# Optimization experiments

Hardware: AMD Instinct MI355X
Metric: run time of the kernel (lower is better)

## Reference

```python
import jax, jax.numpy as jnp
import numpy as np

L, C, B = 256, 20, 1024


def _pos_mask(L):
    # pairwise mask: l2 - l1 >= 1, shape (L, L); broadcast over channels
    ls = jnp.arange(L)
    return (ls[None, :] - ls[:, None]) >= 1


def setup_inputs() -> dict:
    key = jax.random.key(0)
    k0, k1, k2 = jax.random.split(key, 3)
    x_lc = jax.random.uniform(k0, (B, L, C), dtype=jnp.float32)
    theta_0 = jnp.zeros((1,), dtype=jnp.float32)
    theta_lc = jax.random.normal(k1, (1, L, C), dtype=jnp.float32) / np.sqrt(L)
    pm = _pos_mask(L)
    theta_lclc = (jax.random.normal(k2, (1, L, C, L, C), dtype=jnp.float32)
                  / np.sqrt(L * L)) * pm[None, :, None, :, None]
    mask = pm
    return {"x_lc": x_lc, "theta_0": theta_0, "theta_lc": theta_lc,
            "theta_lclc": theta_lclc, "mask": mask}


def reference(x_lc, theta_0, theta_lc, theta_lclc, mask):
    Bn = x_lc.shape[0]
    # additive term: sum_{l,c} theta_lc * x
    phi = theta_0 + jnp.einsum('blc,zlc->b', x_lc, theta_lc)[:, None]
    # pairwise term as a masked bilinear form: x^T (mask * theta) x
    # (avoids materializing the (B,L,C,L,C) broadcast of the original)
    theta_m = theta_lclc[0] * mask[:, None, :, None].astype(theta_lclc.dtype)
    LC = L * C
    xf = x_lc.reshape(Bn, LC)                      # (B, LC)
    tf_ = theta_m.reshape(LC, LC)                  # (LC, LC)
    pair = jnp.einsum('bi,ij,bj->b', xf, tf_, xf)  # two GEMMs under the hood
    phi = phi + pair[:, None]
    return phi
```

## Files before the change

kernel.cpp:

```cpp
#include <hip/hip_runtime.h>
#include <stdint.h>

#define LDIM 256
#define CDIM 20
#define LC   5120
#define NB   1024
#define BM   128
#define BN   256
#define ITOT64 1640

typedef __attribute__((ext_vector_type(8))) short short8;
typedef __attribute__((ext_vector_type(4))) float float4v;
typedef __attribute__((ext_vector_type(4))) unsigned int uint4v;
typedef unsigned short ushort_t;

#define TB_BYTES (52428800ull)
#define XB_BYTES (10485760ull)
#define WS_NEED  (TB_BYTES + XB_BYTES)

__device__ inline uint32_t pack_bf16x2(float a, float b) {
    uint32_t ua = __float_as_uint(a);
    uint32_t ub = __float_as_uint(b);
    ua += 0x7fffu + ((ua >> 16) & 1u);
    ub += 0x7fffu + ((ub >> 16) & 1u);
    return (ua >> 16) | (ub & 0xffff0000u);
}

__device__ inline float bf16_to_f32(ushort_t u) {
    return __uint_as_float(((uint32_t)u) << 16);
}

__device__ inline void load_lds16(const void* g, void* l) {
    __builtin_amdgcn_global_load_lds(
        (const __attribute__((address_space(1))) uint32_t*)g,
        (__attribute__((address_space(3))) uint32_t*)l, 16, 0, 0);
}

__global__ __launch_bounds__(256) void conv_kernel(
    const float* __restrict__ T, const float* __restrict__ X,
    const float* __restrict__ th0, const float* __restrict__ thlc,
    ushort_t* __restrict__ Tb, ushort_t* __restrict__ Xb,
    float* __restrict__ out)
{
    const int bid = blockIdx.x;
    const int t   = threadIdx.x;
    __shared__ float red[4];

    if (bid < LC) {
        const int r  = bid;
        const int tk = (r >> 7) << 7;
        const float*  src = T  + (size_t)r * LC;
        ushort_t*     dst = Tb + (size_t)r * LC;
        for (int c = tk + t * 4; c < LC; c += 1024) {
            float4 f = *(const float4*)(src + c);
            uint2 u;
            u.x = pack_bf16x2(f.x, f.y);
            u.y = pack_bf16x2(f.z, f.w);
            *(uint2*)(dst + c) = u;
        }
    } else {
        const int b = bid - LC;
        const float*  src = X  + (size_t)b * LC;
        ushort_t*     dst = Xb + (size_t)b * LC;
        float s = 0.f;
        for (int c = t * 4; c < LC; c += 1024) {
            float4 f = *(const float4*)(src + c);
            float4 w = *(const float4*)(thlc + c);
            s += f.x * w.x + f.y * w.y + f.z * w.z + f.w * w.w;
            uint2 u;
            u.x = pack_bf16x2(f.x, f.y);
            u.y = pack_bf16x2(f.z, f.w);
            *(uint2*)(dst + c) = u;
        }
        s += __shfl_xor(s, 1);  s += __shfl_xor(s, 2);  s += __shfl_xor(s, 4);
        s += __shfl_xor(s, 8);  s += __shfl_xor(s, 16); s += __shfl_xor(s, 32);
        if ((t & 63) == 0) red[t >> 6] = s;
        __syncthreads();
        if (t == 0) out[b] = th0[0] + red[0] + red[1] + red[2] + red[3];
    }
}

__global__ __launch_bounds__(256, 2) void pair_bf(
    const ushort_t* __restrict__ Tb, const ushort_t* __restrict__ Xb,
    float* __restrict__ out)
{
    const int n    = blockIdx.x;
    const int kblk = (n & 7) | (((n >> 5) & 15) << 3);
    const int bn0  = ((n >> 3) & 3) * BN;

    const int gbeg = (ITOT64 * kblk) >> 7;
    const int gend = (ITOT64 * (kblk + 1)) >> 7;

    int it = 0, pre = 0;
    while (pre + (80 - 2 * it) <= gbeg) { pre += 80 - 2 * it; ++it; }
    int li = gbeg - pre;

    __shared__ __align__(16) ushort_t A_s[1024 * 8];
    __shared__ __align__(16) ushort_t B_s[2048 * 8];

    const int t    = threadIdx.x;
    const int lane = t & 63;
    const int wid  = t >> 6;
    const int wm   = (wid >> 1) * 64;
    const int wn   = (wid & 1) * 128;
    const int l16  = lane & 15;
    const int qk   = lane >> 4;

    uint32_t offA[4];
    #pragma unroll
    for (int j = 0; j < 4; ++j) {
        const int c = (wid << 8) + (j << 6) + lane;
        const int row = c >> 3;
        const int g = (c & 7) ^ (row & 7);
        offA[j] = (uint32_t)row * LC + (g << 3);
    }
    uint32_t offB[8];
    #pragma unroll
    for (int j = 0; j < 8; ++j) {
        const int c = (wid << 9) + (j << 6) + lane;
        const int row = c >> 3;
        const int g = (c & 7) ^ (row & 7);
        offB[j] = (uint32_t)(bn0 + row) * LC + (g << 3);
    }

    int adrA[2][4], adrB[2][8];
    #pragma unroll
    for (int step = 0; step < 2; ++step) {
        const int kf = step * 4 + qk;
        #pragma unroll
        for (int mt = 0; mt < 4; ++mt) {
            const int r = wm + mt * 16 + l16;
            adrA[step][mt] = ((r << 3) + (kf ^ (r & 7))) << 4;
        }
        #pragma unroll
        for (int nt = 0; nt < 8; ++nt) {
            const int r = wn + nt * 16 + l16;
            adrB[step][nt] = ((r << 3) + (kf ^ (r & 7))) << 4;
        }
    }

    int   i0    = it << 7;
    int   k0    = i0 + (li << 6);
    size_t baseA = (size_t)i0 * LC + k0;

    float4v acc[4][8];
    #pragma unroll
    for (int mt = 0; mt < 4; ++mt)
        #pragma unroll
        for (int nt = 0; nt < 8; ++nt)
            #pragma unroll
            for (int r = 0; r < 4; ++r) acc[mt][nt][r] = 0.f;

    for (int g = gbeg; g < gend; ++g) {
        __syncthreads();
        #pragma unroll
        for (int j = 0; j < 4; ++j)
            load_lds16(Tb + baseA + offA[j], A_s + (((wid << 8) + (j << 6)) << 3));
        #pragma unroll
        for (int j = 0; j < 8; ++j)
            load_lds16(Xb + k0 + offB[j],   B_s + (((wid << 9) + (j << 6)) << 3));
        __syncthreads();

        #pragma unroll
        for (int step = 0; step < 2; ++step) {
            short8 af[4], bfr[8];
            #pragma unroll
            for (int mt = 0; mt < 4; ++mt)
                af[mt] = *(const short8*)((const char*)A_s + adrA[step][mt]);
            #pragma unroll
            for (int nt = 0; nt < 8; ++nt)
                bfr[nt] = *(const short8*)((const char*)B_s + adrB[step][nt]);
            #pragma unroll
            for (int mt = 0; mt < 4; ++mt)
                #pragma unroll
                for (int nt = 0; nt < 8; ++nt)
                    acc[mt][nt] = __builtin_amdgcn_mfma_f32_16x16x32_bf16(
                        af[mt], bfr[nt], acc[mt][nt], 0, 0, 0);
        }

        ++li;
        const bool segEnd = (li == 80 - 2 * it);
        if (segEnd || g + 1 == gend) {
            #pragma unroll
            for (int nt = 0; nt < 8; ++nt) {
                const int b = bn0 + wn + nt * 16 + l16;
                const ushort_t* xb = Xb + (size_t)b * LC + i0 + wm + qk * 4;
                float s = 0.f;
                #pragma unroll
                for (int mt = 0; mt < 4; ++mt) {
                    ushort4 xv = *(const ushort4*)(xb + mt * 16);
                    s += acc[mt][nt][0] * bf16_to_f32(xv.x)
                       + acc[mt][nt][1] * bf16_to_f32(xv.y)
                       + acc[mt][nt][2] * bf16_to_f32(xv.z)
                       + acc[mt][nt][3] * bf16_to_f32(xv.w);
                }
                s += __shfl_xor(s, 16);
                s += __shfl_xor(s, 32);
                if (qk == 0) atomicAdd(&out[b], s);
            }
            #pragma unroll
            for (int mt = 0; mt < 4; ++mt)
                #pragma unroll
                for (int nt = 0; nt < 8; ++nt)
                    #pragma unroll
                    for (int r = 0; r < 4; ++r) acc[mt][nt][r] = 0.f;
        }
        if (segEnd) {
            ++it; li = 0;
            if (it < 40) {
                i0 = it << 7;
                k0 = i0;
                baseA = (size_t)i0 * LC + k0;
            }
        } else {
            k0 += 64;
            baseA += 64;
        }
    }
}

__global__ __launch_bounds__(256) void init_kernel(
    const float* __restrict__ x, const float* __restrict__ th0,
    const float* __restrict__ thlc, float* __restrict__ out)
{
    const int b = blockIdx.x;
    const float4* xb = (const float4*)(x + (size_t)b * LC);
    const float4* tv = (const float4*)thlc;
    float s = 0.f;
    for (int i = threadIdx.x; i < LC / 4; i += 256) {
        float4 a = xb[i], t = tv[i];
        s += a.x * t.x + a.y * t.y + a.z * t.z + a.w * t.w;
    }
    s += __shfl_xor(s, 1);  s += __shfl_xor(s, 2);  s += __shfl_xor(s, 4);
    s += __shfl_xor(s, 8);  s += __shfl_xor(s, 16); s += __shfl_xor(s, 32);
    __shared__ float red[4];
    if ((threadIdx.x & 63) == 0) red[threadIdx.x >> 6] = s;
    __syncthreads();
    if (threadIdx.x == 0) out[b] = th0[0] + red[0] + red[1] + red[2] + red[3];
}

__global__ __launch_bounds__(256) void pair_kernel(
    const float* __restrict__ T, const float* __restrict__ X,
    float* __restrict__ out)
{
    const int n  = blockIdx.x;
    const int r  = n & 7;
    const int g  = n >> 3;
    const int i0  = (g >> 3) * BM;
    const int bn0 = (g & 7) * 128;
    const int kstart = i0;
    const int nIter  = (LC - kstart) >> 6;
    const int ipc    = (nIter + 7) >> 3;
    const int itBeg  = r * ipc;
    const int itEnd  = (itBeg + ipc < nIter) ? (itBeg + ipc) : nIter;
    if (itBeg >= itEnd) return;
    const int kbeg   = kstart + (itBeg << 6);

    __shared__ __align__(16) short A_s[8 * BM * 8];
    __shared__ __align__(16) short B_s[8 * BM * 8];

    const int t    = threadIdx.x;
    const int lane = t & 63;
    const int wid  = t >> 6;
    const int wm   = (wid >> 1) * 64;
    const int wn   = (wid & 1) * 64;
    const int l16  = lane & 15;
    const int qk   = lane >> 4;

    const float* pA[4]; const float* pB[4]; int sIdx[4];
    #pragma unroll
    for (int u = 0; u < 4; ++u) {
        const int id  = t + u * 256;
        const int row = id >> 3;
        const int kq  = id & 7;
        pA[u] = T + (size_t)(i0 + row) * LC + kbeg + kq * 8;
        pB[u] = X + (size_t)(bn0 + row) * LC + kbeg + kq * 8;
        sIdx[u] = (kq * BM + (row ^ kq)) * 8;
    }

    float4v acc[4][4] = {};
    for (int itr = itBeg; itr < itEnd; ++itr) {
        __syncthreads();
        #pragma unroll
        for (int u = 0; u < 4; ++u) {
            float4 a0 = ((const float4*)pA[u])[0];
            float4 a1 = ((const float4*)pA[u])[1];
            float4 b0 = ((const float4*)pB[u])[0];
            float4 b1 = ((const float4*)pB[u])[1];
            pA[u] += 64; pB[u] += 64;
            uint4v va, vb;
            va[0] = pack_bf16x2(a0.x, a0.y); va[1] = pack_bf16x2(a0.z, a0.w);
            va[2] = pack_bf16x2(a1.x, a1.y); va[3] = pack_bf16x2(a1.z, a1.w);
            vb[0] = pack_bf16x2(b0.x, b0.y); vb[1] = pack_bf16x2(b0.z, b0.w);
            vb[2] = pack_bf16x2(b1.x, b1.y); vb[3] = pack_bf16x2(b1.z, b1.w);
            *(uint4v*)(A_s + sIdx[u]) = va;
            *(uint4v*)(B_s + sIdx[u]) = vb;
        }
        __syncthreads();
        #pragma unroll
        for (int step = 0; step < 2; ++step) {
            const int kf = step * 4 + qk;
            short8 af[4], bfr[4];
            #pragma unroll
            for (int mt = 0; mt < 4; ++mt)
                af[mt] = *(const short8*)(A_s + (kf * BM + ((wm + mt * 16 + l16) ^ kf)) * 8);
            #pragma unroll
            for (int nt = 0; nt < 4; ++nt)
                bfr[nt] = *(const short8*)(B_s + (kf * BM + ((wn + nt * 16 + l16) ^ kf)) * 8);
            #pragma unroll
            for (int mt = 0; mt < 4; ++mt)
                #pragma unroll
                for (int nt = 0; nt < 4; ++nt)
                    acc[mt][nt] = __builtin_amdgcn_mfma_f32_16x16x32_bf16(
                        af[mt], bfr[nt], acc[mt][nt], 0, 0, 0);
        }
    }
    #pragma unroll
    for (int nt = 0; nt < 4; ++nt) {
        const int b = bn0 + wn + nt * 16 + l16;
        const float* xb = X + (size_t)b * LC + i0 + wm + qk * 4;
        float s = 0.f;
        #pragma unroll
        for (int mt = 0; mt < 4; ++mt) {
            float4 xv = *(const float4*)(xb + mt * 16);
            s += acc[mt][nt][0] * xv.x + acc[mt][nt][1] * xv.y +
                 acc[mt][nt][2] * xv.z + acc[mt][nt][3] * xv.w;
        }
        s += __shfl_xor(s, 16);
        s += __shfl_xor(s, 32);
        if (qk == 0) atomicAdd(&out[b], s);
    }
}

extern "C" void kernel_launch(void* const* d_in, const int* in_sizes, int n_in,
                              void* d_out, int out_size, void* d_ws, size_t ws_size,
                              hipStream_t stream) {
    const float* x    = (const float*)d_in[0];
    const float* th0  = (const float*)d_in[1];
    const float* thlc = (const float*)d_in[2];
    const float* T    = (const float*)d_in[3];
    float* out = (float*)d_out;

    if (ws_size >= WS_NEED) {
        ushort_t* Tb = (ushort_t*)d_ws;
        ushort_t* Xb = (ushort_t*)((char*)d_ws + TB_BYTES);
        conv_kernel<<<LC + NB, 256, 0, stream>>>(T, x, th0, thlc, Tb, Xb, out);
        pair_bf<<<512, 256, 0, stream>>>(Tb, Xb, out);
    } else {
        init_kernel<<<NB, 256, 0, stream>>>(x, th0, thlc, out);
        pair_kernel<<<(LC / BM) * (NB / 128) * 8, 256, 0, stream>>>(T, x, out);
    }
}
```

Measured before the change: 215.5 us.

## Fuse fp32-to-bf16 conversion of theta into the pairwise GEMM tile loads

Drops the separate pass that converted the theta matrix to a bf16 workspace copy. The GEMM kernel now loads fp32 theta tiles into registers, packs them to bf16 and stores them swizzled into LDS. This removes a large write and reread of the bf16 copy and shrinks the workspace. In exchange, each column block rereads fp32 data at twice the byte width, and the asynchronous direct-to-LDS loads for A are replaced by synchronous register staging.

```diff
diff --git a/kernel.cpp b/kernel.cpp
--- a/kernel.cpp
+++ b/kernel.cpp
@@ -14,9 +14,8 @@
 typedef __attribute__((ext_vector_type(4))) unsigned int uint4v;
 typedef unsigned short ushort_t;
 
-#define TB_BYTES (52428800ull)
 #define XB_BYTES (10485760ull)
-#define WS_NEED  (TB_BYTES + XB_BYTES)
+#define WS_NEED  (XB_BYTES)
 
 __device__ inline uint32_t pack_bf16x2(float a, float b) {
     uint32_t ua = __float_as_uint(a);
@@ -36,52 +35,36 @@
         (__attribute__((address_space(3))) uint32_t*)l, 16, 0, 0);
 }
 
-__global__ __launch_bounds__(256) void conv_kernel(
-    const float* __restrict__ T, const float* __restrict__ X,
-    const float* __restrict__ th0, const float* __restrict__ thlc,
-    ushort_t* __restrict__ Tb, ushort_t* __restrict__ Xb,
+__global__ __launch_bounds__(256) void xconv_kernel(
+    const float* __restrict__ X, const float* __restrict__ th0,
+    const float* __restrict__ thlc, ushort_t* __restrict__ Xb,
     float* __restrict__ out)
 {
-    const int bid = blockIdx.x;
-    const int t   = threadIdx.x;
+    const int b = blockIdx.x;
+    const int t = threadIdx.x;
     __shared__ float red[4];
 
-    if (bid < LC) {
-        const int r  = bid;
-        const int tk = (r >> 7) << 7;
-        const float*  src = T  + (size_t)r * LC;
-        ushort_t*     dst = Tb + (size_t)r * LC;
-        for (int c = tk + t * 4; c < LC; c += 1024) {
-            float4 f = *(const float4*)(src + c);
-            uint2 u;
-            u.x = pack_bf16x2(f.x, f.y);
-            u.y = pack_bf16x2(f.z, f.w);
-            *(uint2*)(dst + c) = u;
-        }
-    } else {
-        const int b = bid - LC;
-        const float*  src = X  + (size_t)b * LC;
-        ushort_t*     dst = Xb + (size_t)b * LC;
-        float s = 0.f;
-        for (int c = t * 4; c < LC; c += 1024) {
-            float4 f = *(const float4*)(src + c);
-            float4 w = *(const float4*)(thlc + c);
-            s += f.x * w.x + f.y * w.y + f.z * w.z + f.w * w.w;
-            uint2 u;
-            u.x = pack_bf16x2(f.x, f.y);
-            u.y = pack_bf16x2(f.z, f.w);
-            *(uint2*)(dst + c) = u;
-        }
-        s += __shfl_xor(s, 1);  s += __shfl_xor(s, 2);  s += __shfl_xor(s, 4);
-        s += __shfl_xor(s, 8);  s += __shfl_xor(s, 16); s += __shfl_xor(s, 32);
-        if ((t & 63) == 0) red[t >> 6] = s;
-        __syncthreads();
-        if (t == 0) out[b] = th0[0] + red[0] + red[1] + red[2] + red[3];
-    }
-}
-
-__global__ __launch_bounds__(256, 2) void pair_bf(
-    const ushort_t* __restrict__ Tb, const ushort_t* __restrict__ Xb,
+    const float*  src = X  + (size_t)b * LC;
+    ushort_t*     dst = Xb + (size_t)b * LC;
+    float s = 0.f;
+    for (int c = t * 4; c < LC; c += 1024) {
+        float4 f = *(const float4*)(src + c);
+        float4 w = *(const float4*)(thlc + c);
+        s += f.x * w.x + f.y * w.y + f.z * w.z + f.w * w.w;
+        uint2 u;
+        u.x = pack_bf16x2(f.x, f.y);
+        u.y = pack_bf16x2(f.z, f.w);
+        *(uint2*)(dst + c) = u;
+    }
+    s += __shfl_xor(s, 1);  s += __shfl_xor(s, 2);  s += __shfl_xor(s, 4);
+    s += __shfl_xor(s, 8);  s += __shfl_xor(s, 16); s += __shfl_xor(s, 32);
+    if ((t & 63) == 0) red[t >> 6] = s;
+    __syncthreads();
+    if (t == 0) out[b] = th0[0] + red[0] + red[1] + red[2] + red[3];
+}
+
+__global__ __launch_bounds__(256, 2) void pair_fused(
+    const float* __restrict__ T, const ushort_t* __restrict__ Xb,
     float* __restrict__ out)
 {
     const int n    = blockIdx.x;
@@ -106,14 +89,17 @@
     const int l16  = lane & 15;
     const int qk   = lane >> 4;
 
-    uint32_t offA[4];
+    const int r32 = t >> 3;
+    const int ga  = t & 7;
+    uint32_t offTa[4];
+    int      wAdr[4];
     #pragma unroll
     for (int j = 0; j < 4; ++j) {
-        const int c = (wid << 8) + (j << 6) + lane;
-        const int row = c >> 3;
-        const int g = (c & 7) ^ (row & 7);
-        offA[j] = (uint32_t)row * LC + (g << 3);
-    }
+        const int row = r32 + j * 32;
+        offTa[j] = (uint32_t)row * LC + (ga << 3);
+        wAdr[j]  = ((row << 3) + (ga ^ (row & 7))) << 4;
+    }
+
     uint32_t offB[8];
     #pragma unroll
     for (int j = 0; j < 8; ++j) {
@@ -139,9 +125,8 @@
         }
     }
 
-    int   i0    = it << 7;
-    int   k0    = i0 + (li << 6);
-    size_t baseA = (size_t)i0 * LC + k0;
+    int i0 = it << 7;
+    int k0 = i0 + (li << 6);
 
     float4v acc[4][8];
     #pragma unroll
@@ -153,12 +138,26 @@
 
     for (int g = gbeg; g < gend; ++g) {
         __syncthreads();
-        #pragma unroll
-        for (int j = 0; j < 4; ++j)
-            load_lds16(Tb + baseA + offA[j], A_s + (((wid << 8) + (j << 6)) << 3));
+
+        const float* Tbase = T + (size_t)i0 * LC + k0;
+        float4 a0[4], a1[4];
+        #pragma unroll
+        for (int j = 0; j < 4; ++j) {
+            a0[j] = *(const float4*)(Tbase + offTa[j]);
+            a1[j] = *(const float4*)(Tbase + offTa[j] + 4);
+        }
         #pragma unroll
         for (int j = 0; j < 8; ++j)
-            load_lds16(Xb + k0 + offB[j],   B_s + (((wid << 9) + (j << 6)) << 3));
+            load_lds16(Xb + k0 + offB[j], B_s + (((wid << 9) + (j << 6)) << 3));
+        #pragma unroll
+        for (int j = 0; j < 4; ++j) {
+            uint4v v;
+            v[0] = pack_bf16x2(a0[j].x, a0[j].y);
+            v[1] = pack_bf16x2(a0[j].z, a0[j].w);
+            v[2] = pack_bf16x2(a1[j].x, a1[j].y);
+            v[3] = pack_bf16x2(a1[j].z, a1[j].w);
+            *(uint4v*)((char*)A_s + wAdr[j]) = v;
+        }
         __syncthreads();
 
         #pragma unroll
@@ -210,11 +209,9 @@
             if (it < 40) {
                 i0 = it << 7;
                 k0 = i0;
-                baseA = (size_t)i0 * LC + k0;
             }
         } else {
             k0 += 64;
-            baseA += 64;
         }
     }
 }
@@ -342,10 +339,9 @@
     float* out = (float*)d_out;
 
     if (ws_size >= WS_NEED) {
-        ushort_t* Tb = (ushort_t*)d_ws;
-        ushort_t* Xb = (ushort_t*)((char*)d_ws + TB_BYTES);
-        conv_kernel<<<LC + NB, 256, 0, stream>>>(T, x, th0, thlc, Tb, Xb, out);
-        pair_bf<<<512, 256, 0, stream>>>(Tb, Xb, out);
+        ushort_t* Xb = (ushort_t*)d_ws;
+        xconv_kernel<<<NB, 256, 0, stream>>>(x, th0, thlc, Xb, out);
+        pair_fused<<<512, 256, 0, stream>>>(T, Xb, out);
     } else {
         init_kernel<<<NB, 256, 0, stream>>>(x, th0, thlc, out);
         pair_kernel<<<(LC / BM) * (NB / 128) * 8, 256, 0, stream>>>(T, x, out);
```

Result: faster. 205.0 us (-4.9%).

## Replace LDS-staged bf16 GEMM with direct-to-register per-wave MFMA tiles

Applied to the files above, without the earlier changes.

The bf16 pair kernel no longer stages A/B tiles through LDS with block-wide barriers. Each wave now loads MFMA fragments straight from global memory into registers and works on a 64x64 tile with its own slice of the triangular K range. The triangle granularity drops from 128 to 64 rows, so the conversion kernel skips more of the masked lower triangle. Occupancy is raised to three blocks per CU. This removes barrier and LDS overhead, but in exchange there is no data reuse across waves, more redundant global/L2 traffic, and uncoalesced 16-byte row loads.

```diff
diff --git a/kernel.cpp b/kernel.cpp
--- a/kernel.cpp
+++ b/kernel.cpp
@@ -5,13 +5,10 @@
 #define CDIM 20
 #define LC   5120
 #define NB   1024
-#define BM   128
-#define BN   256
-#define ITOT64 1640
+#define ITOT 3240
 
 typedef __attribute__((ext_vector_type(8))) short short8;
 typedef __attribute__((ext_vector_type(4))) float float4v;
-typedef __attribute__((ext_vector_type(4))) unsigned int uint4v;
 typedef unsigned short ushort_t;
 
 #define TB_BYTES (52428800ull)
@@ -28,12 +25,6 @@
 
 __device__ inline float bf16_to_f32(ushort_t u) {
     return __uint_as_float(((uint32_t)u) << 16);
-}
-
-__device__ inline void load_lds16(const void* g, void* l) {
-    __builtin_amdgcn_global_load_lds(
-        (const __attribute__((address_space(1))) uint32_t*)g,
-        (__attribute__((address_space(3))) uint32_t*)l, 16, 0, 0);
 }
 
 __global__ __launch_bounds__(256) void conv_kernel(
@@ -48,7 +39,7 @@
 
     if (bid < LC) {
         const int r  = bid;
-        const int tk = (r >> 7) << 7;
+        const int tk = (r >> 6) << 6;
         const float*  src = T  + (size_t)r * LC;
         ushort_t*     dst = Tb + (size_t)r * LC;
         for (int c = tk + t * 4; c < LC; c += 1024) {
@@ -80,111 +71,76 @@
     }
 }
 
-__global__ __launch_bounds__(256, 2) void pair_bf(
+__global__ __launch_bounds__(256, 3) void pair_direct(
     const ushort_t* __restrict__ Tb, const ushort_t* __restrict__ Xb,
     float* __restrict__ out)
 {
-    const int n    = blockIdx.x;
-    const int kblk = (n & 7) | (((n >> 5) & 15) << 3);
-    const int bn0  = ((n >> 3) & 3) * BN;
-
-    const int gbeg = (ITOT64 * kblk) >> 7;
-    const int gend = (ITOT64 * (kblk + 1)) >> 7;
+    const int bid   = blockIdx.x;
+    const int btile = bid & 15;
+    const int bn0   = btile << 6;
+    const int wid   = threadIdx.x >> 6;
+    const int lane  = threadIdx.x & 63;
+    const int c     = ((bid >> 4) << 2) + wid;
+
+    const int gbeg = (ITOT * c) >> 8;
+    const int gend = (ITOT * (c + 1)) >> 8;
 
     int it = 0, pre = 0;
-    while (pre + (80 - 2 * it) <= gbeg) { pre += 80 - 2 * it; ++it; }
+    while (pre + (80 - it) <= gbeg) { pre += 80 - it; ++it; }
     int li = gbeg - pre;
 
-    __shared__ __align__(16) ushort_t A_s[1024 * 8];
-    __shared__ __align__(16) ushort_t B_s[2048 * 8];
-
-    const int t    = threadIdx.x;
-    const int lane = t & 63;
-    const int wid  = t >> 6;
-    const int wm   = (wid >> 1) * 64;
-    const int wn   = (wid & 1) * 128;
-    const int l16  = lane & 15;
-    const int qk   = lane >> 4;
-
-    uint32_t offA[4];
-    #pragma unroll
-    for (int j = 0; j < 4; ++j) {
-        const int c = (wid << 8) + (j << 6) + lane;
-        const int row = c >> 3;
-        const int g = (c & 7) ^ (row & 7);
-        offA[j] = (uint32_t)row * LC + (g << 3);
-    }
-    uint32_t offB[8];
-    #pragma unroll
-    for (int j = 0; j < 8; ++j) {
-        const int c = (wid << 9) + (j << 6) + lane;
-        const int row = c >> 3;
-        const int g = (c & 7) ^ (row & 7);
-        offB[j] = (uint32_t)(bn0 + row) * LC + (g << 3);
-    }
-
-    int adrA[2][4], adrB[2][8];
-    #pragma unroll
-    for (int step = 0; step < 2; ++step) {
-        const int kf = step * 4 + qk;
-        #pragma unroll
-        for (int mt = 0; mt < 4; ++mt) {
-            const int r = wm + mt * 16 + l16;
-            adrA[step][mt] = ((r << 3) + (kf ^ (r & 7))) << 4;
-        }
-        #pragma unroll
-        for (int nt = 0; nt < 8; ++nt) {
-            const int r = wn + nt * 16 + l16;
-            adrB[step][nt] = ((r << 3) + (kf ^ (r & 7))) << 4;
-        }
-    }
-
-    int   i0    = it << 7;
-    int   k0    = i0 + (li << 6);
-    size_t baseA = (size_t)i0 * LC + k0;
-
-    float4v acc[4][8];
+    const int l16 = lane & 15;
+    const int qk  = lane >> 4;
+
+    uint32_t offA[4], offBf[4];
     #pragma unroll
     for (int mt = 0; mt < 4; ++mt)
-        #pragma unroll
-        for (int nt = 0; nt < 8; ++nt)
+        offA[mt] = (uint32_t)(mt * 16 + l16) * LC + qk * 8;
+    #pragma unroll
+    for (int nt = 0; nt < 4; ++nt)
+        offBf[nt] = (uint32_t)(bn0 + nt * 16 + l16) * LC + qk * 8;
+
+    int i0 = it << 6;
+    int k0 = i0 + (li << 6);
+
+    float4v acc[4][4];
+    #pragma unroll
+    for (int mt = 0; mt < 4; ++mt)
+        #pragma unroll
+        for (int nt = 0; nt < 4; ++nt)
             #pragma unroll
             for (int r = 0; r < 4; ++r) acc[mt][nt][r] = 0.f;
 
     for (int g = gbeg; g < gend; ++g) {
-        __syncthreads();
-        #pragma unroll
-        for (int j = 0; j < 4; ++j)
-            load_lds16(Tb + baseA + offA[j], A_s + (((wid << 8) + (j << 6)) << 3));
-        #pragma unroll
-        for (int j = 0; j < 8; ++j)
-            load_lds16(Xb + k0 + offB[j],   B_s + (((wid << 9) + (j << 6)) << 3));
-        __syncthreads();
-
-        #pragma unroll
-        for (int step = 0; step < 2; ++step) {
-            short8 af[4], bfr[8];
-            #pragma unroll
-            for (int mt = 0; mt < 4; ++mt)
-                af[mt] = *(const short8*)((const char*)A_s + adrA[step][mt]);
-            #pragma unroll
-            for (int nt = 0; nt < 8; ++nt)
-                bfr[nt] = *(const short8*)((const char*)B_s + adrB[step][nt]);
+        const ushort_t* Ab = Tb + (size_t)i0 * LC + k0;
+        const ushort_t* Bb = Xb + k0;
+
+        short8 af[2][4], bfr[2][4];
+        #pragma unroll
+        for (int s = 0; s < 2; ++s) {
+            #pragma unroll
+            for (int mt = 0; mt < 4; ++mt)
+                af[s][mt] = *(const short8*)(Ab + offA[mt] + s * 32);
+            #pragma unroll
+            for (int nt = 0; nt < 4; ++nt)
+                bfr[s][nt] = *(const short8*)(Bb + offBf[nt] + s * 32);
+        }
+        #pragma unroll
+        for (int s = 0; s < 2; ++s)
             #pragma unroll
             for (int mt = 0; mt < 4; ++mt)
                 #pragma unroll
-                for (int nt = 0; nt < 8; ++nt)
+                for (int nt = 0; nt < 4; ++nt)
                     acc[mt][nt] = __builtin_amdgcn_mfma_f32_16x16x32_bf16(
-                        af[mt], bfr[nt], acc[mt][nt], 0, 0, 0);
-        }
+                        af[s][mt], bfr[s][nt], acc[mt][nt], 0, 0, 0);
 
         ++li;
-        const bool segEnd = (li == 80 - 2 * it);
+        const bool segEnd = (li == 80 - it);
         if (segEnd || g + 1 == gend) {
             #pragma unroll
-            for (int nt = 0; nt < 8; ++nt) {
-                const int b = bn0 + wn + nt * 16 + l16;
-                const ushort_t* xb = Xb + (size_t)b * LC + i0 + wm + qk * 4;
+            for (int nt = 0; nt < 4; ++nt) {
+                const int b = bn0 + nt * 16 + l16;
+                const ushort_t* xb = Xb + (size_t)b * LC + i0 + qk * 4;
                 float s = 0.f;
                 #pragma unroll
                 for (int mt = 0; mt < 4; ++mt) {
@@ -201,20 +157,16 @@
             #pragma unroll
             for (int mt = 0; mt < 4; ++mt)
                 #pragma unroll
-                for (int nt = 0; nt < 8; ++nt)
+                for (int nt = 0; nt < 4; ++nt)
                     #pragma unroll
                     for (int r = 0; r < 4; ++r) acc[mt][nt][r] = 0.f;
         }
         if (segEnd) {
             ++it; li = 0;
-            if (it < 40) {
-                i0 = it << 7;
-                k0 = i0;
-                baseA = (size_t)i0 * LC + k0;
-            }
+            i0 = it << 6;
+            k0 = i0;
         } else {
             k0 += 64;
-            baseA += 64;
         }
     }
 }
@@ -239,6 +191,7 @@
     if (threadIdx.x == 0) out[b] = th0[0] + red[0] + red[1] + red[2] + red[3];
 }
 
+#define BM 128
 __global__ __launch_bounds__(256) void pair_kernel(
     const float* __restrict__ T, const float* __restrict__ X,
     float* __restrict__ out)
@@ -278,6 +231,7 @@
         sIdx[u] = (kq * BM + (row ^ kq)) * 8;
     }
 
+    typedef __attribute__((ext_vector_type(4))) unsigned int uint4v;
     float4v acc[4][4] = {};
     for (int itr = itBeg; itr < itEnd; ++itr) {
         __syncthreads();
@@ -345,7 +299,7 @@
         ushort_t* Tb = (ushort_t*)d_ws;
         ushort_t* Xb = (ushort_t*)((char*)d_ws + TB_BYTES);
         conv_kernel<<<LC + NB, 256, 0, stream>>>(T, x, th0, thlc, Tb, Xb, out);
-        pair_bf<<<512, 256, 0, stream>>>(Tb, Xb, out);
+        pair_direct<<<1024, 256, 0, stream>>>(Tb, Xb, out);
     } else {
         init_kernel<<<NB, 256, 0, stream>>>(x, th0, thlc, out);
         pair_kernel<<<(LC / BM) * (NB / 128) * 8, 256, 0, stream>>>(T, x, out);
```

After: 282.8 us. 31.2% more time.
